# Kernel tuning notes

Hardware: AMD Instinct MI355X
Metric: run time of the kernel (lower is better)

Reference implementation:

```python
import jax, jax.numpy as jnp
import numpy as np

N_HEADS = 32
N_KV_HEADS = 8
HEAD_DIM = 64
D_MODEL = 2048
EPS = 1e-6
THETA = 10000.0


def _rms_norm(x, w):
    # normalize over last dim (head_dim)
    norm = jax.lax.rsqrt(jnp.mean(jnp.square(x), axis=-1, keepdims=True) + EPS)
    return x * norm * w


def _rope(x):
    # x: (B, H, T, D)
    T, D = x.shape[2], x.shape[3]
    inv_freq = 1.0 / (THETA ** (jnp.arange(0, D, 2, dtype=jnp.float32) / D))
    t = jnp.arange(T, dtype=jnp.float32)
    freqs = jnp.outer(t, inv_freq)                      # (T, D/2)
    freqs = jnp.concatenate([freqs, freqs], axis=-1)    # (T, D)
    cos = jnp.cos(freqs)[None, None]                    # (1,1,T,D)
    sin = jnp.sin(freqs)[None, None]
    x1, x2 = x[..., : D // 2], x[..., D // 2 :]
    x_rot = jnp.concatenate([-x2, x1], axis=-1)
    return x * cos + x_rot * sin


def setup_inputs() -> dict:
    key = jax.random.key(0)
    ks = jax.random.split(key, 5)
    B, T = 2, 2048
    s = 0.02
    return {
        "x": jax.random.normal(ks[0], (B, T, D_MODEL), jnp.float32),
        "wq": jax.random.normal(ks[1], (D_MODEL, D_MODEL), jnp.float32) * s,
        "wk": jax.random.normal(ks[2], (N_KV_HEADS * HEAD_DIM, D_MODEL), jnp.float32) * s,
        "wv": jax.random.normal(ks[3], (N_KV_HEADS * HEAD_DIM, D_MODEL), jnp.float32) * s,
        "wo": jax.random.normal(ks[4], (D_MODEL, D_MODEL), jnp.float32) * s,
        "q_norm_w": jnp.ones((HEAD_DIM,), jnp.float32),
        "k_norm_w": jnp.ones((HEAD_DIM,), jnp.float32),
    }


def reference(x, wq, wk, wv, wo, q_norm_w, k_norm_w):
    B, T, C = x.shape
    G = N_HEADS // N_KV_HEADS

    q = (x @ wq.T).reshape(B, T, N_HEADS, HEAD_DIM).transpose(0, 2, 1, 3)      # (B,H,T,D)
    k = (x @ wk.T).reshape(B, T, N_KV_HEADS, HEAD_DIM).transpose(0, 2, 1, 3)   # (B,KH,T,D)
    v = (x @ wv.T).reshape(B, T, N_KV_HEADS, HEAD_DIM).transpose(0, 2, 1, 3)

    q = _rms_norm(q, q_norm_w)
    k = _rms_norm(k, k_norm_w)

    q = _rope(q)
    k = _rope(k)

    # GQA head-expand: each kv head repeated G times consecutively
    k = jnp.repeat(k, G, axis=1)   # (B,H,T,D)
    v = jnp.repeat(v, G, axis=1)

    scale = 1.0 / np.sqrt(HEAD_DIM)
    scores = jnp.einsum("bhqd,bhkd->bhqk", q, k) * scale
    causal = jnp.tril(jnp.ones((T, T), dtype=bool))
    scores = jnp.where(causal[None, None], scores, jnp.finfo(scores.dtype).min)
    attn = jax.nn.softmax(scores, axis=-1)
    out = jnp.einsum("bhqk,bhkd->bhqd", attn, v)   # (B,H,T,D)

    out = out.transpose(0, 2, 1, 3).reshape(B, T, C)
    return out @ wo.T
```

## Files before the change

kernel.cpp:

```cpp
#include <hip/hip_runtime.h>

typedef __bf16 bf16;
typedef __bf16 bf16x8 __attribute__((ext_vector_type(8)));
typedef float f32x4 __attribute__((ext_vector_type(4)));

#define DEV __device__ __forceinline__

DEV void gload16(const void* g, void* l) {
  __builtin_amdgcn_global_load_lds(
      (__attribute__((address_space(1))) void*)g,
      (__attribute__((address_space(3))) void*)l,
      16, 0, 0);
}

DEV unsigned pack_bf16(float a, float b) {
  union { bf16 h[2]; unsigned u; } u;
  u.h[0] = (bf16)a; u.h[1] = (bf16)b;
  return u.u;
}

__global__ __launch_bounds__(256) void cvt_fused(
    const float* __restrict__ s0, const float* __restrict__ s1,
    const float* __restrict__ s2, const float* __restrict__ s3,
    const float* __restrict__ s4, bf16* __restrict__ out) {
  const long i = ((long)blockIdx.x * 256 + threadIdx.x) * 8;
  const float* src;
  long off;
  if (i < 8388608)       { src = s0; off = i; }
  else if (i < 12582912) { src = s1; off = i - 8388608; }
  else if (i < 13631488) { src = s2; off = i - 12582912; }
  else if (i < 14680064) { src = s3; off = i - 13631488; }
  else                   { src = s4; off = i - 14680064; }
  const float4* p = (const float4*)(src + off);
  float4 a = p[0], b = p[1];
  bf16x8 o;
  o[0] = (bf16)a.x; o[1] = (bf16)a.y; o[2] = (bf16)a.z; o[3] = (bf16)a.w;
  o[4] = (bf16)b.x; o[5] = (bf16)b.y; o[6] = (bf16)b.z; o[7] = (bf16)b.w;
  *(bf16x8*)(out + i) = o;
}

__global__ __launch_bounds__(256) void rope_table(float2* __restrict__ tab) {
  const int idx = blockIdx.x * 256 + threadIdx.x;
  const int t = idx >> 5, fi = idx & 31;
  const float invf = expf(-(float)fi * (9.210340371976184f / 32.0f));
  float sn, cs;
  sincosf((float)t * invf, &sn, &cs);
  tab[idx] = make_float2(cs, sn);
}

template <typename OutT>
__global__ __launch_bounds__(512, 2) void gemm8p(
    const bf16* __restrict__ A, const bf16* __restrict__ B, OutT* __restrict__ C,
    int M, int N, int K) {
  __shared__ bf16 As[2][256 * 64];
  __shared__ bf16 Bs[2][256 * 64];
  const int tid = threadIdx.x;
  const int lane = tid & 63;
  const int wv = tid >> 6;
  const int wm = wv >> 2, wn = wv & 3;
  const int l15 = lane & 15, l4 = lane >> 4;
  const int swz7 = l15 & 7;

  const int nx = gridDim.x;
  const int nwg = nx * gridDim.y;
  int wg = blockIdx.y * nx + blockIdx.x;
  wg = (wg & 7) * (nwg >> 3) + (wg >> 3);
  const long m0 = (long)(wg / nx) * 256;
  const long n0 = (long)(wg % nx) * 256;
  const int NT = K >> 6;

  f32x4 acc[8][4];
#pragma unroll
  for (int i = 0; i < 8; ++i)
#pragma unroll
    for (int j = 0; j < 4; ++j) acc[i][j] = (f32x4){0.f, 0.f, 0.f, 0.f};

  auto stageA = [&](int t, int q) {
#pragma unroll
    for (int it = 0; it < 2; ++it) {
      const int c = it * 512 + tid;
      const int row = ((c >> 9) << 7) + q * 64 + ((c >> 3) & 63);
      const int cc = c & 7;
      gload16(A + (m0 + row) * (long)K + t * 64 + ((cc ^ (row & 7)) << 3),
              &As[t & 1][row * 64 + cc * 8]);
    }
  };
  auto stageB = [&](int t, int q) {
#pragma unroll
    for (int it = 0; it < 2; ++it) {
      const int c = it * 512 + tid;
      const int row = ((c >> 8) << 6) + q * 32 + ((c >> 3) & 31);
      const int cc = c & 7;
      gload16(B + (n0 + row) * (long)K + t * 64 + ((cc ^ (row & 7)) << 3),
              &Bs[t & 1][row * 64 + cc * 8]);
    }
  };

#define PHASE(CUR, QM, QN, STAGE, VM) do {                                      \
    __builtin_amdgcn_sched_barrier(0);                                          \
    bf16x8 af_[2][4], bf_[2][2];                                                \
    _Pragma("unroll")                                                           \
    for (int kk = 0; kk < 2; ++kk) {                                            \
      _Pragma("unroll")                                                         \
      for (int i = 0; i < 4; ++i)                                               \
        af_[kk][i] = *(const bf16x8*)&As[CUR][                                  \
            (wm * 128 + (QM) * 64 + i * 16 + l15) * 64 +                        \
            (((kk * 4 + l4) ^ swz7) << 3)];                                     \
      _Pragma("unroll")                                                         \
      for (int j = 0; j < 2; ++j)                                               \
        bf_[kk][j] = *(const bf16x8*)&Bs[CUR][                                  \
            (wn * 64 + (QN) * 32 + j * 16 + l15) * 64 +                         \
            (((kk * 4 + l4) ^ swz7) << 3)];                                     \
    }                                                                           \
    STAGE;                                                                      \
    VM;                                                                         \
    __builtin_amdgcn_sched_barrier(0);                                          \
    __builtin_amdgcn_s_barrier();                                               \
    asm volatile("s_waitcnt lgkmcnt(0)" ::: "memory");                          \
    __builtin_amdgcn_sched_barrier(0);                                          \
    __builtin_amdgcn_s_setprio(1);                                              \
    _Pragma("unroll")                                                           \
    for (int kk = 0; kk < 2; ++kk)                                              \
      _Pragma("unroll")                                                         \
      for (int i = 0; i < 4; ++i)                                               \
        _Pragma("unroll")                                                       \
        for (int j = 0; j < 2; ++j)                                             \
          acc[(QM) * 4 + i][(QN) * 2 + j] =                                     \
              __builtin_amdgcn_mfma_f32_16x16x32_bf16(                          \
                  af_[kk][i], bf_[kk][j], acc[(QM) * 4 + i][(QN) * 2 + j],      \
                  0, 0, 0);                                                     \
    __builtin_amdgcn_s_setprio(0);                                              \
    __builtin_amdgcn_s_barrier();                                               \
  } while (0)

  stageA(0, 0); stageA(0, 1); stageB(0, 0); stageB(0, 1);
  stageA(1, 0); stageB(1, 0);
  asm volatile("s_waitcnt vmcnt(4)" ::: "memory");
  __builtin_amdgcn_sched_barrier(0);
  __builtin_amdgcn_s_barrier();

  for (int T = 0; T < NT - 2; ++T) {
    const int cur = T & 1;
    PHASE(cur, 0, 0, stageA(T + 1, 1), );
    PHASE(cur, 0, 1, stageB(T + 1, 1), );
    PHASE(cur, 1, 0, stageA(T + 2, 0), );
    PHASE(cur, 1, 1, stageB(T + 2, 0),
          asm volatile("s_waitcnt vmcnt(4)" ::: "memory"));
  }
  {
    const int cur = (NT - 2) & 1;
    PHASE(cur, 0, 0, stageA(NT - 1, 1), );
    PHASE(cur, 0, 1, stageB(NT - 1, 1), );
    PHASE(cur, 1, 0, , );
    PHASE(cur, 1, 1, , asm volatile("s_waitcnt vmcnt(0)" ::: "memory"));
  }
  {
    const int cur = (NT - 1) & 1;
    PHASE(cur, 0, 0, , );
    PHASE(cur, 0, 1, , );
    PHASE(cur, 1, 0, , );
    PHASE(cur, 1, 1, , );
  }
#undef PHASE

#pragma unroll
  for (int i = 0; i < 8; ++i)
#pragma unroll
    for (int j = 0; j < 4; ++j) {
      const long row = m0 + wm * 128 + i * 16 + l4 * 4;
      const long col = n0 + wn * 64 + j * 16 + l15;
#pragma unroll
      for (int r = 0; r < 4; ++r)
        C[(row + r) * (long)N + col] = (OutT)acc[i][j][r];
    }
}

__global__ __launch_bounds__(256) void qk_norm_rope(
    const bf16* __restrict__ qkv, const float* __restrict__ qw,
    const float* __restrict__ kw, const float2* __restrict__ tab,
    bf16* __restrict__ Qh, bf16* __restrict__ Kh) {
  const int wg = blockIdx.x * 4 + (threadIdx.x >> 6);
  const int lane = threadIdx.x & 63;
  const int row = wg / 40;
  const int head = wg - row * 40;
  const int b = row >> 11, t = row & 2047;
  const bool is_q = head < 32;
  const int col0 = is_q ? head * 64 : 2048 + (head - 32) * 64;

  float v = (float)qkv[(long)row * 3072 + col0 + lane];
  float ss = v * v;
  ss += __shfl_xor(ss, 1);
  ss += __shfl_xor(ss, 2);
  ss += __shfl_xor(ss, 4);
  ss += __shfl_xor(ss, 8);
  ss += __shfl_xor(ss, 16);
  ss += __shfl_xor(ss, 32);
  const float norm = rsqrtf(ss * (1.0f / 64.0f) + 1e-6f);
  const float* wn = is_q ? qw : kw;
  float xn = v * norm * wn[lane];

  const int fi = lane & 31;
  const float2 cn = tab[t * 32 + fi];
  const float xo = __shfl_xor(xn, 32);
  const float xr = (lane < 32) ? -xo : xo;
  float res = xn * cn.x + xr * cn.y;

  if (is_q) {
    res *= 0.125f;
    Qh[(((long)b * 32 + head) * 2048 + t) * 64 + lane] = (bf16)res;
  } else {
    Kh[(((long)b * 8 + (head - 32)) * 2048 + t) * 64 + lane] = (bf16)res;
  }
}

__global__ __launch_bounds__(256) void v_transpose(
    const bf16* __restrict__ qkv, bf16* __restrict__ Vt) {
  const int bh = blockIdx.x;
  const int t0 = blockIdx.y * 64;
  const int b = bh >> 3, kh = bh & 7;
  __shared__ bf16 tile[64][72];
  const int tid = threadIdx.x;
#pragma unroll
  for (int it = 0; it < 2; ++it) {
    const int tt = it * 32 + (tid >> 3);
    const int d0 = (tid & 7) * 8;
    bf16x8 val = *(const bf16x8*)&qkv[((long)b * 2048 + t0 + tt) * 3072 + 2560 + kh * 64 + d0];
#pragma unroll
    for (int j = 0; j < 8; ++j) tile[tt][d0 + j] = val[j];
  }
  __syncthreads();
#pragma unroll
  for (int it = 0; it < 2; ++it) {
    const int d = it * 32 + (tid >> 3);
    const int tb = (tid & 7) * 8;
    bf16x8 o;
#pragma unroll
    for (int j = 0; j < 8; ++j) o[j] = tile[tb + j][d];
    *(bf16x8*)&Vt[((long)bh * 64 + d) * 2048 + t0 + tb] = o;
  }
}

__global__ __launch_bounds__(256, 4) void attn_fwd(
    const bf16* __restrict__ Q, const bf16* __restrict__ K,
    const bf16* __restrict__ Vt, bf16* __restrict__ O) {
  const int b = blockIdx.x >> 5, h = blockIdx.x & 31;
  const int qb = 31 - (int)blockIdx.y;
  const int q0 = qb * 64;
  const int kvh = h >> 2;
  const bf16* Qp = Q + (((long)b * 32 + h) * 2048 + q0) * 64;
  const bf16* Kp = K + ((long)b * 8 + kvh) * (2048L * 64);
  const bf16* Vp = Vt + ((long)b * 8 + kvh) * (64L * 2048);

  __shared__ bf16 Ks[128 * 64];
  __shared__ bf16 Vs[64 * 128];

  const int tid = threadIdx.x, lane = tid & 63, w = tid >> 6;
  const int l15 = lane & 15, l4 = lane >> 4;
  const int swz7 = l15 & 7;
  const int qwr = q0 + w * 16;
  const int q_g = qwr + l15;

  bf16x8 qf[2];
#pragma unroll
  for (int kk = 0; kk < 2; ++kk)
    qf[kk] = *(const bf16x8*)(Qp + (w * 16 + l15) * 64 + kk * 32 + l4 * 8);

  f32x4 accO[4];
#pragma unroll
  for (int dn = 0; dn < 4; ++dn) accO[dn] = (f32x4){0.f, 0.f, 0.f, 0.f};
  float M = -1e30f, L = 0.f;

  const int NKT = (qb + 2) >> 1;
  for (int kt = 0; kt < NKT; ++kt) {
    const int k0 = kt * 128;
#pragma unroll
    for (int it = 0; it < 4; ++it) {
      const int c = it * 256 + tid;
      const int kr = c >> 3, kc = c & 7;
      gload16(Kp + (long)(k0 + kr) * 64 + ((kc ^ (kr & 7)) << 3), &Ks[c * 8]);
      const int vr = c >> 4, vc = c & 15;
      gload16(Vp + (long)vr * 2048 + k0 + ((vc ^ (vr & 7)) << 3), &Vs[c * 8]);
    }
    __syncthreads();

    f32x4 sT[8];
#pragma unroll
    for (int n = 0; n < 8; ++n) sT[n] = (f32x4){0.f, 0.f, 0.f, 0.f};
#pragma unroll
    for (int kk = 0; kk < 2; ++kk) {
      bf16x8 kf[8];
#pragma unroll
      for (int n = 0; n < 8; ++n)
        kf[n] = *(const bf16x8*)&Ks[(n * 16 + l15) * 64 + (((kk * 4 + l4) ^ swz7) << 3)];
#pragma unroll
      for (int n = 0; n < 8; ++n)
        sT[n] = __builtin_amdgcn_mfma_f32_16x16x32_bf16(kf[n], qf[kk], sT[n], 0, 0, 0);
    }

    if (k0 + 127 > qwr) {
#pragma unroll
      for (int n = 0; n < 8; ++n) {
        const int kbase = k0 + n * 16 + l4 * 4;
#pragma unroll
        for (int r = 0; r < 4; ++r)
          if (kbase + r > q_g) sT[n][r] = -1e30f;
      }
    }

    float pm = -1e30f;
#pragma unroll
    for (int n = 0; n < 8; ++n)
#pragma unroll
      for (int r = 0; r < 4; ++r) pm = fmaxf(pm, sT[n][r]);
    pm = fmaxf(pm, __shfl_xor(pm, 16));
    pm = fmaxf(pm, __shfl_xor(pm, 32));
    if (!__all(pm - M <= 8.0f)) {
      const float newM = fmaxf(M, pm);
      const float sc = __expf(M - newM);
      M = newM;
      L *= sc;
#pragma unroll
      for (int dn = 0; dn < 4; ++dn) accO[dn] *= sc;
    }
    float rs = 0.f;
#pragma unroll
    for (int n = 0; n < 8; ++n)
#pragma unroll
      for (int r = 0; r < 4; ++r) {
        const float pv = __expf(sT[n][r] - M);
        sT[n][r] = pv;
        rs += pv;
      }
    rs += __shfl_xor(rs, 16);
    rs += __shfl_xor(rs, 32);
    L += rs;

    unsigned lo[8], hi[8];
#pragma unroll
    for (int n = 0; n < 8; ++n) {
      lo[n] = pack_bf16(sT[n][0], sT[n][1]);
      hi[n] = pack_bf16(sT[n][2], sT[n][3]);
    }

    const int srcA = l15 | ((l4 & 1) << 5);
    const int srcB = srcA + 16;
    const bool selHi = (l4 >> 1);
#pragma unroll
    for (int kk = 0; kk < 4; ++kk) {
      unsigned d0a = __shfl(lo[2 * kk], srcA), d0b = __shfl(lo[2 * kk + 1], srcA);
      unsigned d1a = __shfl(hi[2 * kk], srcA), d1b = __shfl(hi[2 * kk + 1], srcA);
      unsigned d2a = __shfl(lo[2 * kk], srcB), d2b = __shfl(lo[2 * kk + 1], srcB);
      unsigned d3a = __shfl(hi[2 * kk], srcB), d3b = __shfl(hi[2 * kk + 1], srcB);
      union { unsigned d[4]; bf16x8 v; } pu;
      pu.d[0] = selHi ? d0b : d0a;
      pu.d[1] = selHi ? d1b : d1a;
      pu.d[2] = selHi ? d2b : d2a;
      pu.d[3] = selHi ? d3b : d3a;
      bf16x8 vf[4];
#pragma unroll
      for (int dn = 0; dn < 4; ++dn)
        vf[dn] = *(const bf16x8*)&Vs[(dn * 16 + l15) * 128 + (((kk * 4 + l4) ^ swz7) << 3)];
#pragma unroll
      for (int dn = 0; dn < 4; ++dn)
        accO[dn] = __builtin_amdgcn_mfma_f32_16x16x32_bf16(vf[dn], pu.v, accO[dn], 0, 0, 0);
    }
    __syncthreads();
  }

  const float inv = 1.0f / L;
  const long rowbase = ((long)b * 2048 + q_g) * 2048 + h * 64;
#pragma unroll
  for (int dn = 0; dn < 4; ++dn)
#pragma unroll
    for (int rp = 0; rp < 2; ++rp) {
      const unsigned pk = pack_bf16(accO[dn][2 * rp] * inv, accO[dn][2 * rp + 1] * inv);
      *(unsigned*)&O[rowbase + dn * 16 + l4 * 4 + 2 * rp] = pk;
    }
}

extern "C" void kernel_launch(void* const* d_in, const int* in_sizes, int n_in,
                              void* d_out, int out_size, void* d_ws, size_t ws_size,
                              hipStream_t stream) {
  const float* x   = (const float*)d_in[0];
  const float* wq  = (const float*)d_in[1];
  const float* wk  = (const float*)d_in[2];
  const float* wv  = (const float*)d_in[3];
  const float* wo  = (const float*)d_in[4];
  const float* qnw = (const float*)d_in[5];
  const float* knw = (const float*)d_in[6];
  float* out = (float*)d_out;

  char* ws = (char*)d_ws;
  size_t off = 0;
  auto carve = [&](size_t bytes) -> void* {
    void* p = ws + off;
    off += (bytes + 255) & ~(size_t)255;
    return p;
  };
  bf16* xb    = (bf16*)carve(8388608ull * 2);
  bf16* wqkvb = (bf16*)carve(6291456ull * 2);
  bf16* wob   = (bf16*)carve(4194304ull * 2);
  bf16* qkvb  = (bf16*)carve(12582912ull * 2);
  bf16* Qh    = (bf16*)carve(8388608ull * 2);
  bf16* Kh    = (bf16*)carve(2097152ull * 2);
  bf16* Vt    = (bf16*)carve(2097152ull * 2);
  float2* tab = (float2*)carve(65536ull * 8);

  rope_table<<<256, 256, 0, stream>>>(tab);
  cvt_fused<<<9216, 256, 0, stream>>>(x, wq, wk, wv, wo, xb);

  gemm8p<bf16><<<dim3(12, 16), 512, 0, stream>>>(xb, wqkvb, qkvb, 4096, 3072, 2048);
  qk_norm_rope<<<40960, 256, 0, stream>>>(qkvb, qnw, knw, tab, Qh, Kh);
  v_transpose<<<dim3(16, 32), 256, 0, stream>>>(qkvb, Vt);

  bf16* attnb = xb;
  attn_fwd<<<dim3(64, 32), 256, 0, stream>>>(Qh, Kh, Vt, attnb);

  gemm8p<float><<<dim3(8, 16), 512, 0, stream>>>(attnb, wob, out, 4096, 2048, 2048);
}
```

Baseline: 367.8 us.

## Double-buffer K/V tiles in attention and switch softmax to exp2

Adds a second LDS buffer for K and V tiles so the next tile's global-to-LDS loads are issued before computing on the current tile, with explicit vmcnt waits and barriers. Folds log2(e) into the Q scaling so softmax can use exp2 instead of exp. The doubled shared memory lowers launch-bound occupancy from 4 to 2 blocks per CU, trading parallelism for latency hiding.

```diff
diff --git a/kernel.cpp b/kernel.cpp
--- a/kernel.cpp
+++ b/kernel.cpp
@@ -206,7 +206,7 @@
   float res = xn * cn.x + xr * cn.y;
 
   if (is_q) {
-    res *= 0.125f;
+    res *= 0.18033688011112042f;
     Qh[(((long)b * 32 + head) * 2048 + t) * 64 + lane] = (bf16)res;
   } else {
     Kh[(((long)b * 8 + (head - 32)) * 2048 + t) * 64 + lane] = (bf16)res;
@@ -240,7 +240,7 @@
   }
 }
 
-__global__ __launch_bounds__(256, 4) void attn_fwd(
+__global__ __launch_bounds__(256, 2) void attn_fwd(
     const bf16* __restrict__ Q, const bf16* __restrict__ K,
     const bf16* __restrict__ Vt, bf16* __restrict__ O) {
   const int b = blockIdx.x >> 5, h = blockIdx.x & 31;
@@ -251,8 +251,8 @@
   const bf16* Kp = K + ((long)b * 8 + kvh) * (2048L * 64);
   const bf16* Vp = Vt + ((long)b * 8 + kvh) * (64L * 2048);
 
-  __shared__ bf16 Ks[128 * 64];
-  __shared__ bf16 Vs[64 * 128];
+  __shared__ bf16 Ks[2][128 * 64];
+  __shared__ bf16 Vs[2][64 * 128];
 
   const int tid = threadIdx.x, lane = tid & 63, w = tid >> 6;
   const int l15 = lane & 15, l4 = lane >> 4;
@@ -270,19 +270,34 @@
   for (int dn = 0; dn < 4; ++dn) accO[dn] = (f32x4){0.f, 0.f, 0.f, 0.f};
   float M = -1e30f, L = 0.f;
 
-  const int NKT = (qb + 2) >> 1;
-  for (int kt = 0; kt < NKT; ++kt) {
+  auto stg = [&](int kt, int bsel) {
     const int k0 = kt * 128;
 #pragma unroll
     for (int it = 0; it < 4; ++it) {
       const int c = it * 256 + tid;
       const int kr = c >> 3, kc = c & 7;
-      gload16(Kp + (long)(k0 + kr) * 64 + ((kc ^ (kr & 7)) << 3), &Ks[c * 8]);
+      gload16(Kp + (long)(k0 + kr) * 64 + ((kc ^ (kr & 7)) << 3), &Ks[bsel][c * 8]);
       const int vr = c >> 4, vc = c & 15;
-      gload16(Vp + (long)vr * 2048 + k0 + ((vc ^ (vr & 7)) << 3), &Vs[c * 8]);
-    }
-    __syncthreads();
-
+      gload16(Vp + (long)vr * 2048 + k0 + ((vc ^ (vr & 7)) << 3), &Vs[bsel][c * 8]);
+    }
+  };
+
+  const int NKT = (qb + 2) >> 1;
+  stg(0, 0);
+  for (int kt = 0; kt < NKT; ++kt) {
+    const int cur = kt & 1;
+    __builtin_amdgcn_sched_barrier(0);
+    if (kt + 1 < NKT) {
+      stg(kt + 1, cur ^ 1);
+      asm volatile("s_waitcnt vmcnt(8)" ::: "memory");
+    } else {
+      asm volatile("s_waitcnt vmcnt(0)" ::: "memory");
+    }
+    __builtin_amdgcn_sched_barrier(0);
+    __builtin_amdgcn_s_barrier();
+    __builtin_amdgcn_sched_barrier(0);
+
+    const int k0 = kt * 128;
     f32x4 sT[8];
 #pragma unroll
     for (int n = 0; n < 8; ++n) sT[n] = (f32x4){0.f, 0.f, 0.f, 0.f};
@@ -291,7 +306,7 @@
       bf16x8 kf[8];
 #pragma unroll
       for (int n = 0; n < 8; ++n)
-        kf[n] = *(const bf16x8*)&Ks[(n * 16 + l15) * 64 + (((kk * 4 + l4) ^ swz7) << 3)];
+        kf[n] = *(const bf16x8*)&Ks[cur][(n * 16 + l15) * 64 + (((kk * 4 + l4) ^ swz7) << 3)];
 #pragma unroll
       for (int n = 0; n < 8; ++n)
         sT[n] = __builtin_amdgcn_mfma_f32_16x16x32_bf16(kf[n], qf[kk], sT[n], 0, 0, 0);
@@ -316,7 +331,7 @@
     pm = fmaxf(pm, __shfl_xor(pm, 32));
     if (!__all(pm - M <= 8.0f)) {
       const float newM = fmaxf(M, pm);
-      const float sc = __expf(M - newM);
+      const float sc = exp2f(M - newM);
       M = newM;
       L *= sc;
 #pragma unroll
@@ -327,7 +342,7 @@
     for (int n = 0; n < 8; ++n)
 #pragma unroll
       for (int r = 0; r < 4; ++r) {
-        const float pv = __expf(sT[n][r] - M);
+        const float pv = exp2f(sT[n][r] - M);
         sT[n][r] = pv;
         rs += pv;
       }
@@ -359,12 +374,16 @@
       bf16x8 vf[4];
 #pragma unroll
       for (int dn = 0; dn < 4; ++dn)
-        vf[dn] = *(const bf16x8*)&Vs[(dn * 16 + l15) * 128 + (((kk * 4 + l4) ^ swz7) << 3)];
+        vf[dn] = *(const bf16x8*)&Vs[cur][(dn * 16 + l15) * 128 + (((kk * 4 + l4) ^ swz7) << 3)];
 #pragma unroll
       for (int dn = 0; dn < 4; ++dn)
         accO[dn] = __builtin_amdgcn_mfma_f32_16x16x32_bf16(vf[dn], pu.v, accO[dn], 0, 0, 0);
     }
-    __syncthreads();
+
+    __builtin_amdgcn_sched_barrier(0);
+    asm volatile("s_waitcnt lgkmcnt(0)" ::: "memory");
+    __builtin_amdgcn_sched_barrier(0);
+    __builtin_amdgcn_s_barrier();
   }
 
   const float inv = 1.0f / L;
```

Result: slower. 391.4 us (+6.4%).
